# Optimization experiments

Measured on AMD Instinct MI355X. Metric: run time of the kernel, lower is better.

Reference implementation:

```python
import jax, jax.numpy as jnp
import numpy as np


def setup_inputs() -> dict:
    key = jax.random.key(0)
    k1, k2, k3, k4 = jax.random.split(key, 4)
    HIDDEN = 1024
    L1_CAP = 4096
    L2_CAP = 16384
    B = 4096
    return {
        "query": jax.random.normal(k1, (B, HIDDEN), dtype=jnp.float32),
        "W": jax.random.normal(k2, (HIDDEN, HIDDEN), dtype=jnp.float32) * (1.0 / np.sqrt(HIDDEN)),
        "l1": jax.random.normal(k3, (L1_CAP, HIDDEN), dtype=jnp.float32),
        "l2": jax.random.normal(k4, (L2_CAP, HIDDEN), dtype=jnp.float32),
        "l1_mask": jnp.ones((L1_CAP,), dtype=bool),
        "l2_mask": jnp.ones((L2_CAP,), dtype=bool),
        "top_k": 16,
    }


def reference(query, W, l1, l2, l1_mask, l2_mask, top_k):
    # score_proj: Linear(hidden, hidden, bias=False) -> q @ W.T
    q_proj = query @ W.T                      # [B, H]
    mem = jnp.concatenate([l1, l2], axis=0)   # [M, H]
    mask = jnp.concatenate([l1_mask, l2_mask], axis=0)  # [M]
    # masked scoring
    scores = q_proj @ mem.T                   # [B, M]
    scores = jnp.where(mask[None, :], scores, -jnp.inf)
    # top-k selection + softmax weighting (masks are all True -> k == top_k)
    vals, idx = jax.lax.top_k(scores, top_k)  # [B, K]
    soft = jax.nn.softmax(vals, axis=-1)      # [B, K]
    # gathered memory is detached in the original (mem[idx].detach())
    gathered = jax.lax.stop_gradient(mem)[idx]  # [B, K, H]
    gathered = gathered * soft[..., None]
    return gathered
```

## Files before the change

### kernel.cpp

```cpp
#include <hip/hip_runtime.h>


#define HIDDEN 1024
#define BQ     4096
#define TOPK   16
#define MTOT   20480

typedef __attribute__((ext_vector_type(8)))  short s8v;
typedef __attribute__((ext_vector_type(4)))  float f4v;
typedef __attribute__((ext_vector_type(4)))  int   i4v;
typedef __attribute__((ext_vector_type(8)))  int   i8v;

#define WAITVM(N) asm volatile("s_waitcnt vmcnt(" #N ")" ::: "memory")

static __device__ __forceinline__ unsigned short f32_to_bf16_rne(float f) {
  unsigned u = __float_as_uint(f);
  unsigned r = 0x7FFFu + ((u >> 16) & 1u);
  return (unsigned short)((u + r) >> 16);
}
static __device__ __forceinline__ float bf16_to_f32(unsigned short h) {
  return __uint_as_float(((unsigned)h) << 16);
}

__global__ __launch_bounds__(256) void hm_cvt_split2(
    const float* __restrict__ q, const float* __restrict__ W,
    unsigned short* __restrict__ qh, unsigned short* __restrict__ ql,
    unsigned short* __restrict__ wh, unsigned short* __restrict__ wl) {
  const int NQ = BQ * HIDDEN / 4;
  int i = blockIdx.x * 256 + threadIdx.x;
  const float* in;
  unsigned short *ho, *lo;
  int j;
  if (i < NQ) { in = q; j = i;      ho = qh; lo = ql; }
  else        { in = W; j = i - NQ; ho = wh; lo = wl; }
  float4 x = ((const float4*)in)[j];
  ushort4 h, l;
  h.x = f32_to_bf16_rne(x.x); l.x = f32_to_bf16_rne(x.x - bf16_to_f32(h.x));
  h.y = f32_to_bf16_rne(x.y); l.y = f32_to_bf16_rne(x.y - bf16_to_f32(h.y));
  h.z = f32_to_bf16_rne(x.z); l.z = f32_to_bf16_rne(x.z - bf16_to_f32(h.z));
  h.w = f32_to_bf16_rne(x.w); l.w = f32_to_bf16_rne(x.w - bf16_to_f32(h.w));
  ((ushort4*)ho)[j] = h;
  ((ushort4*)lo)[j] = l;
}

__global__ __launch_bounds__(256) void hm_cvt_fp8(
    const float* __restrict__ in, unsigned char* __restrict__ out8, int n8) {
  int i = blockIdx.x * 256 + threadIdx.x;
  if (i >= n8) return;
  const float4* p = (const float4*)in + (size_t)i * 2;
  float4 x = p[0], y = p[1];
  int u0 = __builtin_amdgcn_cvt_pk_fp8_f32(x.x, x.y, 0, false);
  u0     = __builtin_amdgcn_cvt_pk_fp8_f32(x.z, x.w, u0, true);
  int u1 = __builtin_amdgcn_cvt_pk_fp8_f32(y.x, y.y, 0, false);
  u1     = __builtin_amdgcn_cvt_pk_fp8_f32(y.z, y.w, u1, true);
  uint2 o; o.x = (unsigned)u0; o.y = (unsigned)u1;
  ((uint2*)out8)[i] = o;
}

__global__ __launch_bounds__(256) void hm_cvt_mem_fp8(
    const float* __restrict__ l1, const float* __restrict__ l2,
    unsigned char* __restrict__ out8) {
  int i = blockIdx.x * 256 + threadIdx.x;
  int row = i >> 7, colg = i & 127;
  const float* src = (row < 4096) ? (l1 + (size_t)row * HIDDEN + colg * 8)
                                  : (l2 + (size_t)(row - 4096) * HIDDEN + colg * 8);
  float4 x = ((const float4*)src)[0], y = ((const float4*)src)[1];
  int u0 = __builtin_amdgcn_cvt_pk_fp8_f32(x.x, x.y, 0, false);
  u0     = __builtin_amdgcn_cvt_pk_fp8_f32(x.z, x.w, u0, true);
  int u1 = __builtin_amdgcn_cvt_pk_fp8_f32(y.x, y.y, 0, false);
  u1     = __builtin_amdgcn_cvt_pk_fp8_f32(y.z, y.w, u1, true);
  uint2 o; o.x = (unsigned)u0; o.y = (unsigned)u1;
  ((uint2*)out8)[i] = o;
}

__global__ __launch_bounds__(256) void hm_gemm_split3(
    const unsigned short* __restrict__ Ahi, const unsigned short* __restrict__ Alo,
    const unsigned short* __restrict__ Bhi, const unsigned short* __restrict__ Blo,
    float* __restrict__ Cf, int N, int K) {
  __shared__ unsigned short lds[2][16384];
  const int tid = threadIdx.x, lane = tid & 63, w = tid >> 6;
  const int m0 = blockIdx.x * 128, n0 = blockIdx.y * 128;
  const int wr = (w >> 1) * 64, wc = (w & 1) * 64;
  f4v acc[4][4] = {};
  const unsigned short* plane = (w == 0) ? Ahi : (w == 1) ? Alo : (w == 2) ? Bhi : Blo;
  const int gbase = (w < 2) ? m0 : n0;
  const int kg = lane >> 4, r16 = lane & 15;
  const int NT = K / 32;

  auto STAGE = [&](int cur, int t) {
#pragma unroll
    for (int is = 0; is < 8; ++is) {
      int slot = is * 64 + lane;
      int row = slot >> 2, kgs = slot & 3;
      const unsigned short* gp = plane + (size_t)(gbase + row) * K + (t * 32 + kgs * 8);
      unsigned short* lp = &lds[cur][(w * 512 + is * 64) * 8];
      __builtin_amdgcn_global_load_lds(
          (const __attribute__((address_space(1))) unsigned int*)gp,
          (__attribute__((address_space(3))) unsigned int*)lp, 16, 0, 0);
    }
  };

  STAGE(0, 0);
  __syncthreads();
  for (int t = 0; t < NT; ++t) {
    int cur = t & 1;
    if (t + 1 < NT) STAGE(cur ^ 1, t + 1);

    s8v ah[4], al[4], bh[4], bl[4];
#pragma unroll
    for (int mi = 0; mi < 4; ++mi) {
      int ro = wr + mi * 16 + r16;
      ah[mi] = *(const s8v*)&lds[cur][(0 * 512 + ro * 4 + kg) * 8];
      al[mi] = *(const s8v*)&lds[cur][(1 * 512 + ro * 4 + kg) * 8];
    }
#pragma unroll
    for (int ni = 0; ni < 4; ++ni) {
      int ro = wc + ni * 16 + r16;
      bh[ni] = *(const s8v*)&lds[cur][(2 * 512 + ro * 4 + kg) * 8];
      bl[ni] = *(const s8v*)&lds[cur][(3 * 512 + ro * 4 + kg) * 8];
    }
#pragma unroll
    for (int mi = 0; mi < 4; ++mi)
#pragma unroll
      for (int ni = 0; ni < 4; ++ni) {
        acc[mi][ni] = __builtin_amdgcn_mfma_f32_16x16x32_bf16(ah[mi], bh[ni], acc[mi][ni], 0, 0, 0);
        acc[mi][ni] = __builtin_amdgcn_mfma_f32_16x16x32_bf16(ah[mi], bl[ni], acc[mi][ni], 0, 0, 0);
        acc[mi][ni] = __builtin_amdgcn_mfma_f32_16x16x32_bf16(al[mi], bh[ni], acc[mi][ni], 0, 0, 0);
      }
    __syncthreads();
  }
  const int cr = (lane >> 4) * 4, cc = lane & 15;
#pragma unroll
  for (int mi = 0; mi < 4; ++mi)
#pragma unroll
    for (int ni = 0; ni < 4; ++ni)
#pragma unroll
      for (int j = 0; j < 4; ++j) {
        int R = m0 + wr + mi * 16 + cr + j;
        int Cc = n0 + wc + ni * 16 + cc;
        Cf[(size_t)R * N + Cc] = acc[mi][ni][j];
      }
}

__global__ __launch_bounds__(256, 2) void hm_gemm_fp8(
    const unsigned char* __restrict__ A8, const unsigned char* __restrict__ B8,
    unsigned short* __restrict__ Cbf, int N, int K) {
  __shared__ __align__(16) char smem[65536];
  const int tid = threadIdx.x, lane = tid & 63, w = tid >> 6;
  const int m0 = blockIdx.x * 128, n0 = blockIdx.y * 128;
  const int wr = (w >> 1) * 64, wc = (w & 1) * 64;
  const int r16 = lane & 15, kg = lane >> 4;
  const int sc = 0x7F7F7F7F;
  const int NT = 8;

  f4v acc[4][4] = {};

  const int lrow = lane >> 3;
  const int lkc  = (lane & 7) ^ lrow;

  auto STAGE = [&](int buf, int t) {
    char* bA = smem + buf * 32768;
    char* bB = bA + 16384;
    int k0 = t * 128;
#pragma unroll
    for (int ii = 0; ii < 4; ++ii) {
      int r0 = w * 32 + ii * 8;
      const unsigned char* gA = A8 + (size_t)(m0 + r0 + lrow) * K + k0 + lkc * 16;
      __builtin_amdgcn_global_load_lds(
          (const __attribute__((address_space(1))) unsigned int*)gA,
          (__attribute__((address_space(3))) unsigned int*)(bA + r0 * 128),
          16, 0, 0);
      const unsigned char* gB = B8 + (size_t)(n0 + r0 + lrow) * K + k0 + lkc * 16;
      __builtin_amdgcn_global_load_lds(
          (const __attribute__((address_space(1))) unsigned int*)gB,
          (__attribute__((address_space(3))) unsigned int*)(bB + r0 * 128),
          16, 0, 0);
    }
  };

  STAGE(0, 0);
#pragma unroll
  for (int t = 0; t < NT; ++t) {
    if (t + 1 < NT) { STAGE((t + 1) & 1, t + 1); WAITVM(8); }
    else            { WAITVM(0); }
    __builtin_amdgcn_s_barrier();

    const char* bA = smem + (t & 1) * 32768;
    const char* bB = bA + 16384;
    i8v a[4], b[4];
#pragma unroll
    for (int mi = 0; mi < 4; ++mi) {
      int row = wr + mi * 16 + r16;
      int x = row & 7;
      i4v lo = *(const i4v*)(bA + (row * 8 + ((kg * 2)     ^ x)) * 16);
      i4v hi = *(const i4v*)(bA + (row * 8 + ((kg * 2 + 1) ^ x)) * 16);
      a[mi][0]=lo[0]; a[mi][1]=lo[1]; a[mi][2]=lo[2]; a[mi][3]=lo[3];
      a[mi][4]=hi[0]; a[mi][5]=hi[1]; a[mi][6]=hi[2]; a[mi][7]=hi[3];
    }
#pragma unroll
    for (int ni = 0; ni < 4; ++ni) {
      int row = wc + ni * 16 + r16;
      int x = row & 7;
      i4v lo = *(const i4v*)(bB + (row * 8 + ((kg * 2)     ^ x)) * 16);
      i4v hi = *(const i4v*)(bB + (row * 8 + ((kg * 2 + 1) ^ x)) * 16);
      b[ni][0]=lo[0]; b[ni][1]=lo[1]; b[ni][2]=lo[2]; b[ni][3]=lo[3];
      b[ni][4]=hi[0]; b[ni][5]=hi[1]; b[ni][6]=hi[2]; b[ni][7]=hi[3];
    }
    __builtin_amdgcn_s_setprio(1);
#pragma unroll
    for (int mi = 0; mi < 4; ++mi)
#pragma unroll
      for (int ni = 0; ni < 4; ++ni)
        acc[mi][ni] = __builtin_amdgcn_mfma_scale_f32_16x16x128_f8f6f4(
            a[mi], b[ni], acc[mi][ni], 0, 0, 0, sc, 0, sc);
    __builtin_amdgcn_s_setprio(0);

    asm volatile("s_waitcnt lgkmcnt(0)" ::: "memory");
    __builtin_amdgcn_sched_barrier(0);
    __builtin_amdgcn_s_barrier();
  }

  short* ldsC = (short*)smem;
  const int cr = kg * 4, cc = r16;
#pragma unroll
  for (int mi = 0; mi < 4; ++mi)
#pragma unroll
    for (int ni = 0; ni < 4; ++ni)
#pragma unroll
      for (int j = 0; j < 4; ++j) {
        int row = wr + mi * 16 + cr + j;
        int col = wc + ni * 16 + cc;
        ldsC[row * 128 + col] = (short)f32_to_bf16_rne(acc[mi][ni][j]);
      }
  __syncthreads();
#pragma unroll
  for (int it = 0; it < 8; ++it) {
    int idx = it * 256 + tid;
    int row = idx >> 4, c16 = idx & 15;
    uint4 v = *(const uint4*)(ldsC + row * 128 + c16 * 8);
    *(uint4*)(Cbf + (size_t)(m0 + row) * N + n0 + c16 * 8) = v;
  }
}

__global__ __launch_bounds__(256) void hm_topk(
    const unsigned short* __restrict__ scores, int* __restrict__ stIdx) {
  int tid = threadIdx.x, lane = tid & 63, w = tid >> 6;
  int b = blockIdx.x * 4 + w;
  const uint4* row = (const uint4*)(scores + (size_t)b * MTOT);

  unsigned q[8];
#pragma unroll
  for (int i = 0; i < 8; ++i) q[i] = 0;

  auto push = [&](unsigned p) {
    if (p > q[7]) {
      q[7] = p;
#pragma unroll
      for (int i = 7; i > 0; --i) {
        unsigned hi = q[i - 1] > q[i] ? q[i - 1] : q[i];
        unsigned lo = q[i - 1] > q[i] ? q[i] : q[i - 1];
        q[i - 1] = hi; q[i] = lo;
      }
    }
  };

  for (int it = 0; it < MTOT / 512; ++it) {
    uint4 pk = row[it * 64 + lane];
    unsigned base = (it * 64 + lane) * 8;
    unsigned u4[4] = {pk.x, pk.y, pk.z, pk.w};
#pragma unroll
    for (int j = 0; j < 4; ++j) {
      unsigned v0 = u4[j] & 0xffffu, v1 = u4[j] >> 16;
      unsigned k0 = v0 ^ ((v0 >> 15) ? 0xFFFFu : 0x8000u);
      unsigned k1 = v1 ^ ((v1 >> 15) ? 0xFFFFu : 0x8000u);
      push((k0 << 16) | (base + 2 * j));
      push((k1 << 16) | (base + 2 * j + 1));
    }
  }

  unsigned keep = 0;
#pragma unroll
  for (int r = 0; r < TOPK; ++r) {
    unsigned m = q[0];
#pragma unroll
    for (int mk = 1; mk < 64; mk <<= 1) {
      unsigned o = (unsigned)__shfl_xor((int)m, mk);
      m = m > o ? m : o;
    }
    if (q[0] == m) {
#pragma unroll
      for (int i = 0; i < 7; ++i) q[i] = q[i + 1];
      q[7] = 0;
    }
    if (lane == r) keep = m;
  }
  if (lane < TOPK) stIdx[b * TOPK + lane] = (int)(keep & 0xffffu);
}

__global__ __launch_bounds__(256) void hm_refine_gather(
    const float* __restrict__ qp, const int* __restrict__ stIdx,
    const float* __restrict__ l1, const float* __restrict__ l2,
    float* __restrict__ out) {
  __shared__ float vals[TOPK], wts[TOPK], red[TOPK][4], ssum[1];
  __shared__ int rankOf[TOPK], sidx[TOPK];
  int b = blockIdx.x, tid = threadIdx.x;
  int lane = tid & 63, w = tid >> 6;
  if (tid < TOPK) sidx[tid] = stIdx[b * TOPK + tid];
  float4 q4 = ((const float4*)(qp + (size_t)b * HIDDEN))[tid];
  __syncthreads();

  float4 m4[TOPK];
  float p[TOPK];
#pragma unroll
  for (int k = 0; k < TOPK; ++k) {
    int idx = sidx[k];
    const float4* mr = (idx < 4096) ? (const float4*)(l1 + (size_t)idx * HIDDEN)
                                    : (const float4*)(l2 + (size_t)(idx - 4096) * HIDDEN);
    m4[k] = mr[tid];
    p[k] = q4.x * m4[k].x + q4.y * m4[k].y + q4.z * m4[k].z + q4.w * m4[k].w;
  }
#pragma unroll
  for (int k = 0; k < TOPK; ++k)
#pragma unroll
    for (int mask = 1; mask < 64; mask <<= 1) p[k] += __shfl_xor(p[k], mask);
  if (lane == 0)
#pragma unroll
    for (int k = 0; k < TOPK; ++k) red[k][w] = p[k];
  __syncthreads();
  if (tid < TOPK) vals[tid] = red[tid][0] + red[tid][1] + red[tid][2] + red[tid][3];
  __syncthreads();
  if (tid < TOPK) {
    float vt = vals[tid];
    int it = sidx[tid], r = 0;
    float m = vals[0];
#pragma unroll
    for (int j = 0; j < TOPK; ++j) {
      float vj = vals[j];
      m = fmaxf(m, vj);
      r += (vj > vt || (vj == vt && sidx[j] < it)) ? 1 : 0;
    }
    rankOf[tid] = r;
    wts[tid] = expf(vt - m);
  }
  __syncthreads();
  if (tid == 0) {
    float s = 0.f;
#pragma unroll
    for (int j = 0; j < TOPK; ++j) s += wts[j];
    ssum[0] = s;
  }
  __syncthreads();
  float inv = 1.0f / ssum[0];
#pragma unroll
  for (int k = 0; k < TOPK; ++k) {
    float wt = wts[k] * inv;
    int r = rankOf[k];
    float4 x = m4[k];
    x.x *= wt; x.y *= wt; x.z *= wt; x.w *= wt;
    ((float4*)out)[((size_t)b * TOPK + r) * 256 + tid] = x;
  }
}

extern "C" void kernel_launch(void* const* d_in, const int* in_sizes, int n_in,
                              void* d_out, int out_size, void* d_ws, size_t ws_size,
                              hipStream_t stream) {
  const float* query = (const float*)d_in[0];
  const float* W     = (const float*)d_in[1];
  const float* l1    = (const float*)d_in[2];
  const float* l2    = (const float*)d_in[3];
  float* out = (float*)d_out;

  const size_t MiB = 1024 * 1024;
  char* ws = (char*)d_ws;
  unsigned short* qh  = (unsigned short*)(ws + 0);
  unsigned short* ql  = (unsigned short*)(ws + 8 * MiB);
  unsigned short* wh  = (unsigned short*)(ws + 16 * MiB);
  unsigned short* wl  = (unsigned short*)(ws + 18 * MiB);
  float*          qpf = (float*)(ws + 20 * MiB);
  unsigned char*  qp8 = (unsigned char*)(ws + 0);
  int*            stIdx = (int*)(ws + 36 * MiB);

  unsigned short* scores = (unsigned short*)d_out;
  unsigned char*  mem8   = (unsigned char*)d_out + 200 * MiB;

  hm_cvt_split2<<<dim3((BQ * HIDDEN + HIDDEN * HIDDEN) / 1024), dim3(256), 0, stream>>>(
      query, W, qh, ql, wh, wl);
  hm_gemm_split3<<<dim3(BQ / 128, HIDDEN / 128), dim3(256), 0, stream>>>(
      qh, ql, wh, wl, qpf, HIDDEN, HIDDEN);
  hm_cvt_fp8<<<dim3(BQ * HIDDEN / 2048), dim3(256), 0, stream>>>(qpf, qp8, BQ * HIDDEN / 8);
  hm_cvt_mem_fp8<<<dim3(MTOT * HIDDEN / 2048), dim3(256), 0, stream>>>(l1, l2, mem8);

  hm_gemm_fp8<<<dim3(BQ / 128, MTOT / 128), dim3(256), 0, stream>>>(
      qp8, mem8, scores, MTOT, HIDDEN);
  hm_topk<<<dim3(BQ / 4), dim3(256), 0, stream>>>(scores, stIdx);
  hm_refine_gather<<<dim3(BQ), dim3(256), 0, stream>>>(qpf, stIdx, l1, l2, out);
}
```

Baseline: 307.2 us.

## Prune top-k scan with per-segment maxima from the GEMM epilogue

The fp8 score GEMM epilogue now also computes a per-row maximum for each 128-column segment and writes it to a small segMax buffer. The top-k kernel first picks the 16th-largest segment maximum as a threshold and scans only segments whose maximum reaches it, instead of streaming the full 20480-wide bf16 score row. The two fp8 conversion kernels are also merged into one launch. The cost is extra shuffles and stores in the GEMM epilogue, plus serialized ballot-loop loads in top-k.

```diff
diff --git a/kernel.cpp b/kernel.cpp
--- a/kernel.cpp
+++ b/kernel.cpp
@@ -5,6 +5,7 @@
 #define BQ     4096
 #define TOPK   16
 #define MTOT   20480
+#define NSEG   160
 
 typedef __attribute__((ext_vector_type(8)))  short s8v;
 typedef __attribute__((ext_vector_type(4)))  float f4v;
@@ -20,6 +21,9 @@
 }
 static __device__ __forceinline__ float bf16_to_f32(unsigned short h) {
   return __uint_as_float(((unsigned)h) << 16);
+}
+static __device__ __forceinline__ unsigned bf16_key(unsigned v) {
+  return v ^ ((v >> 15) ? 0xFFFFu : 0x8000u);
 }
 
 __global__ __launch_bounds__(256) void hm_cvt_split2(
@@ -43,34 +47,30 @@
   ((ushort4*)lo)[j] = l;
 }
 
-__global__ __launch_bounds__(256) void hm_cvt_fp8(
-    const float* __restrict__ in, unsigned char* __restrict__ out8, int n8) {
+__global__ __launch_bounds__(256) void hm_cvt_fp8_all(
+    const float* __restrict__ qpf, const float* __restrict__ l1,
+    const float* __restrict__ l2, unsigned char* __restrict__ qp8,
+    unsigned char* __restrict__ mem8) {
+  const int NQ8 = BQ * HIDDEN / 8;
   int i = blockIdx.x * 256 + threadIdx.x;
-  if (i >= n8) return;
-  const float4* p = (const float4*)in + (size_t)i * 2;
-  float4 x = p[0], y = p[1];
-  int u0 = __builtin_amdgcn_cvt_pk_fp8_f32(x.x, x.y, 0, false);
-  u0     = __builtin_amdgcn_cvt_pk_fp8_f32(x.z, x.w, u0, true);
-  int u1 = __builtin_amdgcn_cvt_pk_fp8_f32(y.x, y.y, 0, false);
-  u1     = __builtin_amdgcn_cvt_pk_fp8_f32(y.z, y.w, u1, true);
-  uint2 o; o.x = (unsigned)u0; o.y = (unsigned)u1;
-  ((uint2*)out8)[i] = o;
-}
-
-__global__ __launch_bounds__(256) void hm_cvt_mem_fp8(
-    const float* __restrict__ l1, const float* __restrict__ l2,
-    unsigned char* __restrict__ out8) {
-  int i = blockIdx.x * 256 + threadIdx.x;
-  int row = i >> 7, colg = i & 127;
-  const float* src = (row < 4096) ? (l1 + (size_t)row * HIDDEN + colg * 8)
-                                  : (l2 + (size_t)(row - 4096) * HIDDEN + colg * 8);
+  const float* src;
+  unsigned char* dst;
+  int j;
+  if (i < NQ8) { src = qpf + (size_t)i * 8; dst = qp8; j = i; }
+  else {
+    j = i - NQ8;
+    int row = j >> 7, colg = j & 127;
+    src = (row < 4096) ? (l1 + (size_t)row * HIDDEN + colg * 8)
+                       : (l2 + (size_t)(row - 4096) * HIDDEN + colg * 8);
+    dst = mem8;
+  }
   float4 x = ((const float4*)src)[0], y = ((const float4*)src)[1];
   int u0 = __builtin_amdgcn_cvt_pk_fp8_f32(x.x, x.y, 0, false);
   u0     = __builtin_amdgcn_cvt_pk_fp8_f32(x.z, x.w, u0, true);
   int u1 = __builtin_amdgcn_cvt_pk_fp8_f32(y.x, y.y, 0, false);
   u1     = __builtin_amdgcn_cvt_pk_fp8_f32(y.z, y.w, u1, true);
   uint2 o; o.x = (unsigned)u0; o.y = (unsigned)u1;
-  ((uint2*)out8)[i] = o;
+  ((uint2*)dst)[j] = o;
 }
 
 __global__ __launch_bounds__(256) void hm_gemm_split3(
@@ -144,7 +144,8 @@
 
 __global__ __launch_bounds__(256, 2) void hm_gemm_fp8(
     const unsigned char* __restrict__ A8, const unsigned char* __restrict__ B8,
-    unsigned short* __restrict__ Cbf, int N, int K) {
+    unsigned short* __restrict__ Cbf, unsigned short* __restrict__ segMax,
+    int N, int K) {
   __shared__ __align__(16) char smem[65536];
   const int tid = threadIdx.x, lane = tid & 63, w = tid >> 6;
   const int m0 = blockIdx.x * 128, n0 = blockIdx.y * 128;
@@ -239,14 +240,28 @@
     int row = idx >> 4, c16 = idx & 15;
     uint4 v = *(const uint4*)(ldsC + row * 128 + c16 * 8);
     *(uint4*)(Cbf + (size_t)(m0 + row) * N + n0 + c16 * 8) = v;
+    float m8 = bf16_to_f32((unsigned short)(v.x & 0xffff));
+    m8 = fmaxf(m8, bf16_to_f32((unsigned short)(v.x >> 16)));
+    m8 = fmaxf(m8, bf16_to_f32((unsigned short)(v.y & 0xffff)));
+    m8 = fmaxf(m8, bf16_to_f32((unsigned short)(v.y >> 16)));
+    m8 = fmaxf(m8, bf16_to_f32((unsigned short)(v.z & 0xffff)));
+    m8 = fmaxf(m8, bf16_to_f32((unsigned short)(v.z >> 16)));
+    m8 = fmaxf(m8, bf16_to_f32((unsigned short)(v.w & 0xffff)));
+    m8 = fmaxf(m8, bf16_to_f32((unsigned short)(v.w >> 16)));
+#pragma unroll
+    for (int mask = 1; mask < 16; mask <<= 1) m8 = fmaxf(m8, __shfl_xor(m8, mask));
+    if ((tid & 15) == 0)
+      segMax[(size_t)(m0 + row) * NSEG + (n0 >> 7)] = f32_to_bf16_rne(m8);
   }
 }
 
 __global__ __launch_bounds__(256) void hm_topk(
-    const unsigned short* __restrict__ scores, int* __restrict__ stIdx) {
+    const unsigned short* __restrict__ scores,
+    const unsigned short* __restrict__ segMax, int* __restrict__ stIdx) {
   int tid = threadIdx.x, lane = tid & 63, w = tid >> 6;
   int b = blockIdx.x * 4 + w;
-  const uint4* row = (const uint4*)(scores + (size_t)b * MTOT);
+  const unsigned short* sm = segMax + (size_t)b * NSEG;
+  const unsigned* rowp = (const unsigned*)(scores + (size_t)b * MTOT);
 
   unsigned q[8];
 #pragma unroll
@@ -264,17 +279,46 @@
     }
   };
 
-  for (int it = 0; it < MTOT / 512; ++it) {
-    uint4 pk = row[it * 64 + lane];
-    unsigned base = (it * 64 + lane) * 8;
-    unsigned u4[4] = {pk.x, pk.y, pk.z, pk.w};
-#pragma unroll
-    for (int j = 0; j < 4; ++j) {
-      unsigned v0 = u4[j] & 0xffffu, v1 = u4[j] >> 16;
-      unsigned k0 = v0 ^ ((v0 >> 15) ? 0xFFFFu : 0x8000u);
-      unsigned k1 = v1 ^ ((v1 >> 15) ? 0xFFFFu : 0x8000u);
-      push((k0 << 16) | (base + 2 * j));
-      push((k1 << 16) | (base + 2 * j + 1));
+  unsigned sk[3];
+#pragma unroll
+  for (int g = 0; g < 3; ++g) {
+    int s = g * 64 + lane;
+    sk[g] = (s < NSEG) ? bf16_key(sm[s]) : 0;
+    if (s < NSEG) push((sk[g] << 16) | s);
+  }
+  unsigned tau = 0;
+#pragma unroll
+  for (int r = 0; r < TOPK; ++r) {
+    unsigned m = q[0];
+#pragma unroll
+    for (int mk = 1; mk < 64; mk <<= 1) {
+      unsigned o = (unsigned)__shfl_xor((int)m, mk);
+      m = m > o ? m : o;
+    }
+    if (q[0] == m) {
+#pragma unroll
+      for (int i = 0; i < 7; ++i) q[i] = q[i + 1];
+      q[7] = 0;
+    }
+    tau = m;
+  }
+  tau >>= 16;
+
+#pragma unroll
+  for (int i = 0; i < 8; ++i) q[i] = 0;
+#pragma unroll
+  for (int g = 0; g < 3; ++g) {
+    int s0 = g * 64 + lane;
+    unsigned long long mk = __ballot(s0 < NSEG && sk[g] >= tau);
+    while (mk) {
+      int src = __ffsll(mk) - 1;
+      mk &= mk - 1;
+      int s = g * 64 + src;
+      unsigned d = rowp[s * 64 + lane];
+      unsigned v0 = d & 0xffffu, v1 = d >> 16;
+      int col = s * 128 + lane * 2;
+      push((bf16_key(v0) << 16) | col);
+      push((bf16_key(v1) << 16) | (col + 1));
     }
   }
 
@@ -380,18 +424,19 @@
   unsigned char*  qp8 = (unsigned char*)(ws + 0);
   int*            stIdx = (int*)(ws + 36 * MiB);
 
-  unsigned short* scores = (unsigned short*)d_out;
-  unsigned char*  mem8   = (unsigned char*)d_out + 200 * MiB;
+  unsigned short* scores  = (unsigned short*)d_out;
+  unsigned short* segMax  = (unsigned short*)((char*)d_out + 192 * MiB);
+  unsigned char*  mem8    = (unsigned char*)d_out + 200 * MiB;
 
   hm_cvt_split2<<<dim3((BQ * HIDDEN + HIDDEN * HIDDEN) / 1024), dim3(256), 0, stream>>>(
       query, W, qh, ql, wh, wl);
   hm_gemm_split3<<<dim3(BQ / 128, HIDDEN / 128), dim3(256), 0, stream>>>(
       qh, ql, wh, wl, qpf, HIDDEN, HIDDEN);
-  hm_cvt_fp8<<<dim3(BQ * HIDDEN / 2048), dim3(256), 0, stream>>>(qpf, qp8, BQ * HIDDEN / 8);
-  hm_cvt_mem_fp8<<<dim3(MTOT * HIDDEN / 2048), dim3(256), 0, stream>>>(l1, l2, mem8);
+  hm_cvt_fp8_all<<<dim3((BQ * HIDDEN + MTOT * HIDDEN) / 2048), dim3(256), 0, stream>>>(
+      qpf, l1, l2, qp8, mem8);
 
   hm_gemm_fp8<<<dim3(BQ / 128, MTOT / 128), dim3(256), 0, stream>>>(
-      qp8, mem8, scores, MTOT, HIDDEN);
-  hm_topk<<<dim3(BQ / 4), dim3(256), 0, stream>>>(scores, stIdx);
+      qp8, mem8, scores, segMax, MTOT, HIDDEN);
+  hm_topk<<<dim3(BQ / 4), dim3(256), 0, stream>>>(scores, segMax, stIdx);
   hm_refine_gather<<<dim3(BQ), dim3(256), 0, stream>>>(qpf, stIdx, l1, l2, out);
 }
```

Measured after the change: 278.0 us (median of 2 runs). -9.5%, faster.
